# Kernel tuning notes

Hardware: AMD Instinct MI355X
Metric: run time of the kernel (lower is better)

## Reference

```python
import jax, jax.numpy as jnp
import numpy as np

B, SQ, SK, D = 8, 2048, 2048, 256

def setup_inputs() -> dict:
    key = jax.random.key(0)
    ks = jax.random.split(key, 8)
    x1 = jax.random.normal(ks[0], (B, SQ, D), dtype=jnp.float32)
    x2 = jax.random.normal(ks[1], (B, SK, D), dtype=jnp.float32)
    x3 = jax.random.normal(ks[2], (B, SK, D), dtype=jnp.float32)  # unused by the original forward (value=x3 is dead)
    mask = jax.random.bernoulli(ks[3], 0.8, (B, SK))
    scale = 0.02
    Wq = jax.random.normal(ks[4], (D, D), dtype=jnp.float32) * scale
    Wk = jax.random.normal(ks[5], (D, D), dtype=jnp.float32) * scale
    Wv = jax.random.normal(ks[6], (D, D), dtype=jnp.float32) * scale
    bq = jnp.zeros((D,), jnp.float32)
    bk = jnp.zeros((D,), jnp.float32)
    bv = jnp.zeros((D,), jnp.float32)
    return {"x1": x1, "x2": x2, "x3": x3, "Wq": Wq, "Wk": Wk, "Wv": Wv,
            "bq": bq, "bk": bk, "bv": bv, "mask": mask}

def reference(x1, x2, x3, Wq, Wk, Wv, bq, bk, bv, mask):
    d = x1.shape[-1]
    inv_sqrt_d = 1.0 / jnp.sqrt(jnp.asarray(d, x1.dtype))
    # Projections (single-head MHA with query scaling, as in torch MHA internals)
    q = (x1 @ Wq + bq) * inv_sqrt_d          # [B, SQ, D]
    k = x2 @ Wk + bk                          # [B, SK, D]
    v = x2 @ Wv + bv                          # forward_value(key): value projected from key input
    # Raw scores
    qk = jnp.einsum('bqd,bkd->bqk', q, k)     # [B, SQ, SK]
    # Mask-derived per-column rescale: qk /= (mask.size(0)/mask.sum(-2))**0.5
    m = mask.astype(qk.dtype)                 # [B, SK]
    col_count = jnp.sum(m, axis=0, keepdims=True)           # [1, SK]
    factor = jnp.sqrt(jnp.asarray(mask.shape[0], qk.dtype) / col_count)  # [1, SK]
    qk = qk / factor                          # broadcast over [B, SQ, SK]; div-by-inf -> 0 where column count is 0
    attn = jax.nn.softmax(qk, axis=-1)
    # dropout is identity in eval / p=0
    out = jnp.einsum('bqk,bkd->bqd', attn, v)  # [B, SQ, D]
    return out
```

## Files before the change

### kernel.cpp

```cpp
#include <hip/hip_runtime.h>
#include <hip/hip_bf16.h>
#include <math.h>

#define B_  8
#define SQ_ 2048
#define SK_ 2048
#define D_  256
#define NSPLIT 4
#define KEYS_PER_SPLIT (SK_ / NSPLIT)
#define NT (KEYS_PER_SPLIT / 32)

typedef __attribute__((ext_vector_type(8))) short bf16x8;
typedef __attribute__((ext_vector_type(4))) float f32x4;
typedef __attribute__((ext_vector_type(4))) unsigned short u16x4;
typedef __attribute__((ext_vector_type(8))) _Float16 f16x8;

static __device__ __forceinline__ unsigned short f2bf(float f) {
    unsigned int u = __builtin_bit_cast(unsigned int, f);
    u += 0x7FFFu + ((u >> 16) & 1u);
    return (unsigned short)(u >> 16);
}

static __device__ __forceinline__ void gld_lds16(const unsigned short* g, unsigned short* l) {
    __builtin_amdgcn_global_load_lds(
        (const __attribute__((address_space(1))) unsigned int*)g,
        (__attribute__((address_space(3))) unsigned int*)l, 16, 0, 0);
}

__global__ void prep_kernel(const float* __restrict__ Wq, const float* __restrict__ Wk,
                            const float* __restrict__ Wv, const int* __restrict__ mask,
                            unsigned short* __restrict__ wT, float* __restrict__ r) {
    int bid = blockIdx.x;
    if (bid < 768) {
        int p = bid >> 8, k = bid & 255, n = threadIdx.x;
        const float* W = (p == 0 ? Wq : (p == 1 ? Wk : Wv));
        wT[(size_t)p * D_ * D_ + (size_t)n * D_ + k] = f2bf(W[(size_t)k * D_ + n]);
    } else {
        int s = (bid - 768) * 256 + threadIdx.x;
        float c = 0.f;
#pragma unroll
        for (int b = 0; b < B_; b++) c += (mask[b * SK_ + s] != 0) ? 1.f : 0.f;
        r[s] = sqrtf(c * 0.125f);
    }
}

__global__ __launch_bounds__(256) void proj_kernel(
    const float* __restrict__ x1, const float* __restrict__ x2,
    const float* __restrict__ bq, const float* __restrict__ bk, const float* __restrict__ bv,
    const unsigned short* __restrict__ wT, const float* __restrict__ r,
    unsigned short* __restrict__ qb, unsigned short* __restrict__ kb,
    unsigned short* __restrict__ vt)
{
    __shared__ unsigned short xs[64][264];
    __shared__ unsigned short wsh[256][36];
    const int tid = threadIdx.x;
    const int mt = blockIdx.x, b = blockIdx.y, p = blockIdx.z;
    const int m0 = mt * 64;
    const float* x = (p == 0 ? x1 : x2) + (size_t)b * SQ_ * D_;

#pragma unroll
    for (int i = 0; i < 16; i++) {
        int id = tid + i * 256;
        int row = id >> 6, c4 = id & 63;
        float4 v = *(const float4*)(x + (size_t)(m0 + row) * D_ + c4 * 4);
        u16x4 u;
        u.x = f2bf(v.x); u.y = f2bf(v.y); u.z = f2bf(v.z); u.w = f2bf(v.w);
        *(u16x4*)(&xs[row][c4 * 4]) = u;
    }

    const int wv = tid >> 6, lane = tid & 63, l15 = lane & 15, quad = lane >> 4;
    const unsigned short* w = wT + (size_t)p * D_ * D_ + (size_t)tid * D_;

    f32x4 acc[4][4];
#pragma unroll
    for (int a = 0; a < 4; a++)
#pragma unroll
        for (int n = 0; n < 4; n++) acc[a][n] = (f32x4){0.f, 0.f, 0.f, 0.f};

    bf16x8 Wreg[4];
#pragma unroll
    for (int j = 0; j < 4; j++) Wreg[j] = *(const bf16x8*)(w + j * 8);

    for (int c = 0; c < 8; c++) {
        __syncthreads();
#pragma unroll
        for (int j = 0; j < 4; j++) *(bf16x8*)(&wsh[tid][j * 8]) = Wreg[j];
        if (c < 7) {
#pragma unroll
            for (int j = 0; j < 4; j++) Wreg[j] = *(const bf16x8*)(w + (c + 1) * 32 + j * 8);
        }
        __syncthreads();

        bf16x8 af[4];
#pragma unroll
        for (int a = 0; a < 4; a++)
            af[a] = *(const bf16x8*)(&xs[a * 16 + l15][c * 32 + quad * 8]);
#pragma unroll
        for (int nt = 0; nt < 4; nt++) {
            bf16x8 bfr = *(const bf16x8*)(&wsh[wv * 64 + nt * 16 + l15][quad * 8]);
#pragma unroll
            for (int a = 0; a < 4; a++)
                acc[a][nt] = __builtin_amdgcn_mfma_f32_16x16x32_bf16(af[a], bfr, acc[a][nt], 0, 0, 0);
        }
    }

    const float* bias = (p == 0 ? bq : (p == 1 ? bk : bv));
    if (p == 2) {
#pragma unroll
        for (int nt = 0; nt < 4; nt++) {
            int d = wv * 64 + nt * 16 + l15;
            float bb = bias[d];
#pragma unroll
            for (int a = 0; a < 4; a++) {
                int seqb = m0 + a * 16 + quad * 4;
                u16x4 u;
#pragma unroll
                for (int g = 0; g < 4; g++) u[g] = f2bf(acc[a][nt][g] + bb);
                *(u16x4*)(vt + ((size_t)b * D_ + d) * SK_ + seqb) = u;
            }
        }
    } else {
        unsigned short* dst = (p == 0 ? qb : kb);
#pragma unroll
        for (int a = 0; a < 4; a++) {
            int seqb = m0 + a * 16 + quad * 4;
            float rv[4];
#pragma unroll
            for (int g = 0; g < 4; g++)
                rv[g] = (p == 1) ? r[seqb + g] : 0.0625f;
#pragma unroll
            for (int nt = 0; nt < 4; nt++) {
                int col = wv * 64 + nt * 16 + l15;
                float bb = bias[col];
#pragma unroll
                for (int g = 0; g < 4; g++) {
                    float v = (acc[a][nt][g] + bb) * rv[g];
                    dst[((size_t)b * SQ_ + seqb + g) * D_ + col] = f2bf(v);
                }
            }
        }
    }
}

__global__ __launch_bounds__(256, 2) void flash_kernel(
    const unsigned short* __restrict__ qb, const unsigned short* __restrict__ kb,
    const unsigned short* __restrict__ vt, _Float16* __restrict__ Op,
    float* __restrict__ lp)
{
    __shared__ unsigned short Ks[2][32 * 256];
    __shared__ unsigned short Vs[2][256 * 32];
    __shared__ unsigned short Ps[4][32][40];
    const int tid = threadIdx.x;
    const int wv = tid >> 6, lane = tid & 63, l15 = lane & 15, quad = lane >> 4;
    const int bid = blockIdx.x;
    const int g = bid & 31, q = bid >> 5;
    const int b = g >> 2, sp = g & 3;
    const int q0 = q * 128 + wv * 32;

    const unsigned short* kbb = kb + ((size_t)b * SK_ + sp * KEYS_PER_SPLIT) * D_;
    const unsigned short* vtb = vt + (size_t)b * D_ * SK_ + sp * KEYS_PER_SPLIT;

    int krow[4], kck[4], vd[4], vch[4];
#pragma unroll
    for (int i = 0; i < 4; i++) {
        int id = i * 256 + tid;
        krow[i] = id >> 5; kck[i] = (id & 31) ^ (krow[i] & 7);
        vd[i] = id >> 2;   vch[i] = id & 3;
    }

#pragma unroll
    for (int i = 0; i < 4; i++)
        gld_lds16(kbb + (size_t)krow[i] * D_ + kck[i] * 8,
                  &Ks[0][(i * 256 + wv * 64) * 8]);
#pragma unroll
    for (int i = 0; i < 4; i++)
        gld_lds16(vtb + (size_t)vd[i] * SK_ + vch[i] * 8,
                  &Vs[0][(i * 256 + wv * 64) * 8]);

    bf16x8 qf[2][8];
#pragma unroll
    for (int mt = 0; mt < 2; mt++) {
        const unsigned short* qrow = qb + ((size_t)(b * SQ_ + q0 + mt * 16 + l15)) * D_;
#pragma unroll
        for (int c = 0; c < 8; c++)
            qf[mt][c] = *(const bf16x8*)(qrow + c * 32 + quad * 8);
    }

    f32x4 o[2][16];
#pragma unroll
    for (int mt = 0; mt < 2; mt++)
#pragma unroll
        for (int n = 0; n < 16; n++) o[mt][n] = (f32x4){0.f, 0.f, 0.f, 0.f};
    float l_[2][4] = {{0.f, 0.f, 0.f, 0.f}, {0.f, 0.f, 0.f, 0.f}};

    for (int kt = 0; kt < NT; kt++) {
        const int cur = kt & 1;
        __syncthreads();
        if (kt + 1 < NT) {
            const unsigned short* kn = kbb + (size_t)(kt + 1) * 32 * D_;
            const unsigned short* vn = vtb + (size_t)(kt + 1) * 32;
#pragma unroll
            for (int i = 0; i < 4; i++)
                gld_lds16(kn + (size_t)krow[i] * D_ + kck[i] * 8,
                          &Ks[cur ^ 1][(i * 256 + wv * 64) * 8]);
#pragma unroll
            for (int i = 0; i < 4; i++)
                gld_lds16(vn + (size_t)vd[i] * SK_ + vch[i] * 8,
                          &Vs[cur ^ 1][(i * 256 + wv * 64) * 8]);
        }

        f32x4 s[2][2];
        s[0][0] = (f32x4){0.f,0.f,0.f,0.f}; s[0][1] = (f32x4){0.f,0.f,0.f,0.f};
        s[1][0] = (f32x4){0.f,0.f,0.f,0.f}; s[1][1] = (f32x4){0.f,0.f,0.f,0.f};
#pragma unroll
        for (int h = 0; h < 2; h++)
#pragma unroll
            for (int c = 0; c < 8; c++) {
                bf16x8 kf = *(const bf16x8*)(
                    &Ks[cur][(h * 16 + l15) * 256 + (((c * 4 + quad) ^ (l15 & 7)) * 8)]);
                s[0][h] = __builtin_amdgcn_mfma_f32_16x16x32_bf16(qf[0][c], kf, s[0][h], 0, 0, 0);
                s[1][h] = __builtin_amdgcn_mfma_f32_16x16x32_bf16(qf[1][c], kf, s[1][h], 0, 0, 0);
            }

#pragma unroll
        for (int mt = 0; mt < 2; mt++)
#pragma unroll
            for (int h = 0; h < 2; h++)
#pragma unroll
                for (int g2 = 0; g2 < 4; g2++) {
                    float pv = __expf(s[mt][h][g2]);
                    l_[mt][g2] += pv;
                    Ps[wv][mt * 16 + quad * 4 + g2][h * 16 + l15] = f2bf(pv);
                }
        asm volatile("s_waitcnt lgkmcnt(0)" ::: "memory");

        bf16x8 pf0 = *(const bf16x8*)(&Ps[wv][l15][quad * 8]);
        bf16x8 pf1 = *(const bf16x8*)(&Ps[wv][16 + l15][quad * 8]);

#pragma unroll
        for (int n = 0; n < 16; n++) {
            bf16x8 vf = *(const bf16x8*)(&Vs[cur][(n * 16 + l15) * 32 + quad * 8]);
            o[0][n] = __builtin_amdgcn_mfma_f32_16x16x32_bf16(pf0, vf, o[0][n], 0, 0, 0);
            o[1][n] = __builtin_amdgcn_mfma_f32_16x16x32_bf16(pf1, vf, o[1][n], 0, 0, 0);
        }
    }

#pragma unroll
    for (int mt = 0; mt < 2; mt++)
#pragma unroll
        for (int g2 = 0; g2 < 4; g2++) {
            float t = l_[mt][g2];
            t += __shfl_xor(t, 1, 64);
            t += __shfl_xor(t, 2, 64);
            t += __shfl_xor(t, 4, 64);
            t += __shfl_xor(t, 8, 64);
            l_[mt][g2] = t;
        }

    _Float16* op = Op + ((size_t)(sp * B_ + b) * SQ_ + q0) * D_;
#pragma unroll
    for (int mt = 0; mt < 2; mt++)
#pragma unroll
        for (int g2 = 0; g2 < 4; g2++) {
            size_t ro = (size_t)(mt * 16 + quad * 4 + g2) * D_ + l15;
#pragma unroll
            for (int n = 0; n < 16; n++)
                op[ro + n * 16] = (_Float16)(o[mt][n][g2]);
        }
    if (l15 == 0) {
        float* lpp = lp + (size_t)(sp * B_ + b) * SQ_ + q0;
#pragma unroll
        for (int mt = 0; mt < 2; mt++)
#pragma unroll
            for (int g2 = 0; g2 < 4; g2++)
                lpp[mt * 16 + quad * 4 + g2] = l_[mt][g2];
    }
}

__global__ __launch_bounds__(256) void combine_kernel(
    const _Float16* __restrict__ Op, const float* __restrict__ lp,
    float* __restrict__ out)
{
    const int gid = blockIdx.x * 256 + threadIdx.x;
    const int row = gid >> 5;
    const size_t base = (size_t)gid * 8;
    float l = lp[row] + lp[B_ * SQ_ + row] + lp[2 * B_ * SQ_ + row] + lp[3 * B_ * SQ_ + row];
    float inv = 1.f / l;
    float acc[8] = {0,0,0,0,0,0,0,0};
#pragma unroll
    for (int sp = 0; sp < NSPLIT; sp++) {
        f16x8 v = *(const f16x8*)(Op + (size_t)sp * B_ * SQ_ * D_ + base);
#pragma unroll
        for (int j = 0; j < 8; j++) acc[j] += (float)v[j];
    }
    float4 r0 = {acc[0] * inv, acc[1] * inv, acc[2] * inv, acc[3] * inv};
    float4 r1 = {acc[4] * inv, acc[5] * inv, acc[6] * inv, acc[7] * inv};
    *(float4*)(out + base) = r0;
    *(float4*)(out + base + 4) = r1;
}

extern "C" void kernel_launch(void* const* d_in, const int* in_sizes, int n_in,
                              void* d_out, int out_size, void* d_ws, size_t ws_size,
                              hipStream_t stream)
{
    const float* x1 = (const float*)d_in[0];
    const float* x2 = (const float*)d_in[1];
    const float* Wq = (const float*)d_in[3];
    const float* Wk = (const float*)d_in[4];
    const float* Wv = (const float*)d_in[5];
    const float* bq = (const float*)d_in[6];
    const float* bk = (const float*)d_in[7];
    const float* bv = (const float*)d_in[8];
    const int*  mask = (const int*)d_in[9];
    float* out = (float*)d_out;

    char* ws = (char*)d_ws;
    unsigned short* qb = (unsigned short*)(ws);
    unsigned short* kb = (unsigned short*)(ws + 8388608);
    unsigned short* vt = (unsigned short*)(ws + 16777216);
    unsigned short* wT = (unsigned short*)(ws + 25165824);
    float*          r  = (float*)(ws + 25559040);
    float*          lp = (float*)(ws + 25567232);
    _Float16*       Op = (_Float16*)(ws + 25829376);

    prep_kernel<<<dim3(768 + SK_ / 256), 256, 0, stream>>>(Wq, Wk, Wv, mask, wT, r);
    proj_kernel<<<dim3(SQ_ / 64, B_, 3), 256, 0, stream>>>(x1, x2, bq, bk, bv, wT, r, qb, kb, vt);
    flash_kernel<<<dim3((SQ_ / 128) * B_ * NSPLIT), 256, 0, stream>>>(qb, kb, vt, Op, lp);
    combine_kernel<<<dim3((B_ * SQ_ * D_ / 8) / 256), 256, 0, stream>>>(Op, lp, out);
}
```

Before: 188.5 us.

## Rewrite projection as per-wave register GEMM and swizzle V tile in LDS

The projection kernel drops its shared-memory staging and block barriers. Each wave now computes a 16-row by 256-column tile with the activations held in registers, and reads the weight fragments straight from global memory (served from L2/L1). Separately, the flash kernel XOR-swizzles the V tile chunk layout in LDS to reduce bank conflicts on V fragment reads. The trade-off is more global weight traffic and higher register pressure in the projection, in exchange for removing LDS round trips and synchronisation.

```diff
diff --git a/kernel.cpp b/kernel.cpp
--- a/kernel.cpp
+++ b/kernel.cpp
@@ -30,13 +30,13 @@
 __global__ void prep_kernel(const float* __restrict__ Wq, const float* __restrict__ Wk,
                             const float* __restrict__ Wv, const int* __restrict__ mask,
                             unsigned short* __restrict__ wT, float* __restrict__ r) {
-    int bid = blockIdx.x;
+    int bid = blockIdx.x, tid = threadIdx.x;
     if (bid < 768) {
-        int p = bid >> 8, k = bid & 255, n = threadIdx.x;
+        int p = bid >> 8, k = bid & 255;
         const float* W = (p == 0 ? Wq : (p == 1 ? Wk : Wv));
-        wT[(size_t)p * D_ * D_ + (size_t)n * D_ + k] = f2bf(W[(size_t)k * D_ + n]);
+        wT[(size_t)p * D_ * D_ + (size_t)tid * D_ + k] = f2bf(W[(size_t)k * D_ + tid]);
     } else {
-        int s = (bid - 768) * 256 + threadIdx.x;
+        int s = (bid - 768) * 256 + tid;
         float c = 0.f;
 #pragma unroll
         for (int b = 0; b < B_; b++) c += (mask[b * SK_ + s] != 0) ? 1.f : 0.f;
@@ -51,92 +51,74 @@
     unsigned short* __restrict__ qb, unsigned short* __restrict__ kb,
     unsigned short* __restrict__ vt)
 {
-    __shared__ unsigned short xs[64][264];
-    __shared__ unsigned short wsh[256][36];
     const int tid = threadIdx.x;
-    const int mt = blockIdx.x, b = blockIdx.y, p = blockIdx.z;
-    const int m0 = mt * 64;
-    const float* x = (p == 0 ? x1 : x2) + (size_t)b * SQ_ * D_;
-
-#pragma unroll
-    for (int i = 0; i < 16; i++) {
-        int id = tid + i * 256;
-        int row = id >> 6, c4 = id & 63;
-        float4 v = *(const float4*)(x + (size_t)(m0 + row) * D_ + c4 * 4);
-        u16x4 u;
-        u.x = f2bf(v.x); u.y = f2bf(v.y); u.z = f2bf(v.z); u.w = f2bf(v.w);
-        *(u16x4*)(&xs[row][c4 * 4]) = u;
-    }
-
     const int wv = tid >> 6, lane = tid & 63, l15 = lane & 15, quad = lane >> 4;
-    const unsigned short* w = wT + (size_t)p * D_ * D_ + (size_t)tid * D_;
-
-    f32x4 acc[4][4];
-#pragma unroll
-    for (int a = 0; a < 4; a++)
-#pragma unroll
-        for (int n = 0; n < 4; n++) acc[a][n] = (f32x4){0.f, 0.f, 0.f, 0.f};
-
-    bf16x8 Wreg[4];
-#pragma unroll
-    for (int j = 0; j < 4; j++) Wreg[j] = *(const bf16x8*)(w + j * 8);
-
+    const int gw = blockIdx.x * 4 + wv;
+    const int p = gw >> 10;
+    const int idx = gw & 1023;
+    const int b = idx >> 7, s16 = idx & 127;
+    const int row = s16 * 16 + l15;
+
+    const float* x = (p == 0 ? x1 : x2) + ((size_t)b * SQ_ + row) * D_;
+    const unsigned short* wbase = wT + (size_t)p * D_ * D_;
+
+    float4 xa[8], xb[8];
+#pragma unroll
     for (int c = 0; c < 8; c++) {
-        __syncthreads();
-#pragma unroll
-        for (int j = 0; j < 4; j++) *(bf16x8*)(&wsh[tid][j * 8]) = Wreg[j];
-        if (c < 7) {
-#pragma unroll
-            for (int j = 0; j < 4; j++) Wreg[j] = *(const bf16x8*)(w + (c + 1) * 32 + j * 8);
-        }
-        __syncthreads();
-
-        bf16x8 af[4];
-#pragma unroll
-        for (int a = 0; a < 4; a++)
-            af[a] = *(const bf16x8*)(&xs[a * 16 + l15][c * 32 + quad * 8]);
-#pragma unroll
-        for (int nt = 0; nt < 4; nt++) {
-            bf16x8 bfr = *(const bf16x8*)(&wsh[wv * 64 + nt * 16 + l15][quad * 8]);
-#pragma unroll
-            for (int a = 0; a < 4; a++)
-                acc[a][nt] = __builtin_amdgcn_mfma_f32_16x16x32_bf16(af[a], bfr, acc[a][nt], 0, 0, 0);
+        xa[c] = *(const float4*)(x + c * 32 + quad * 8);
+        xb[c] = *(const float4*)(x + c * 32 + quad * 8 + 4);
+    }
+    bf16x8 af[8];
+#pragma unroll
+    for (int c = 0; c < 8; c++) {
+        bf16x8 t;
+        t[0] = (short)f2bf(xa[c].x); t[1] = (short)f2bf(xa[c].y);
+        t[2] = (short)f2bf(xa[c].z); t[3] = (short)f2bf(xa[c].w);
+        t[4] = (short)f2bf(xb[c].x); t[5] = (short)f2bf(xb[c].y);
+        t[6] = (short)f2bf(xb[c].z); t[7] = (short)f2bf(xb[c].w);
+        af[c] = t;
+    }
+
+    f32x4 acc[16];
+#pragma unroll
+    for (int n = 0; n < 16; n++) acc[n] = (f32x4){0.f, 0.f, 0.f, 0.f};
+
+#pragma unroll
+    for (int c = 0; c < 8; c++) {
+#pragma unroll
+        for (int nt = 0; nt < 16; nt++) {
+            bf16x8 wf = *(const bf16x8*)(wbase + (size_t)(nt * 16 + l15) * D_
+                                         + c * 32 + quad * 8);
+            acc[nt] = __builtin_amdgcn_mfma_f32_16x16x32_bf16(af[c], wf, acc[nt], 0, 0, 0);
         }
     }
 
     const float* bias = (p == 0 ? bq : (p == 1 ? bk : bv));
+    const int seqb = s16 * 16 + quad * 4;
     if (p == 2) {
 #pragma unroll
-        for (int nt = 0; nt < 4; nt++) {
-            int d = wv * 64 + nt * 16 + l15;
+        for (int nt = 0; nt < 16; nt++) {
+            int d = nt * 16 + l15;
             float bb = bias[d];
-#pragma unroll
-            for (int a = 0; a < 4; a++) {
-                int seqb = m0 + a * 16 + quad * 4;
-                u16x4 u;
-#pragma unroll
-                for (int g = 0; g < 4; g++) u[g] = f2bf(acc[a][nt][g] + bb);
-                *(u16x4*)(vt + ((size_t)b * D_ + d) * SK_ + seqb) = u;
-            }
+            u16x4 u;
+#pragma unroll
+            for (int g = 0; g < 4; g++) u[g] = f2bf(acc[nt][g] + bb);
+            *(u16x4*)(vt + ((size_t)b * D_ + d) * SK_ + seqb) = u;
         }
     } else {
         unsigned short* dst = (p == 0 ? qb : kb);
-#pragma unroll
-        for (int a = 0; a < 4; a++) {
-            int seqb = m0 + a * 16 + quad * 4;
-            float rv[4];
-#pragma unroll
-            for (int g = 0; g < 4; g++)
-                rv[g] = (p == 1) ? r[seqb + g] : 0.0625f;
-#pragma unroll
-            for (int nt = 0; nt < 4; nt++) {
-                int col = wv * 64 + nt * 16 + l15;
-                float bb = bias[col];
-#pragma unroll
-                for (int g = 0; g < 4; g++) {
-                    float v = (acc[a][nt][g] + bb) * rv[g];
-                    dst[((size_t)b * SQ_ + seqb + g) * D_ + col] = f2bf(v);
-                }
+        float rv[4];
+#pragma unroll
+        for (int g = 0; g < 4; g++)
+            rv[g] = (p == 1) ? r[seqb + g] : 0.0625f;
+#pragma unroll
+        for (int nt = 0; nt < 16; nt++) {
+            int col = nt * 16 + l15;
+            float bb = bias[col];
+#pragma unroll
+            for (int g = 0; g < 4; g++) {
+                float v = (acc[nt][g] + bb) * rv[g];
+                dst[((size_t)b * SQ_ + seqb + g) * D_ + col] = f2bf(v);
             }
         }
     }
@@ -165,17 +147,15 @@
     for (int i = 0; i < 4; i++) {
         int id = i * 256 + tid;
         krow[i] = id >> 5; kck[i] = (id & 31) ^ (krow[i] & 7);
-        vd[i] = id >> 2;   vch[i] = id & 3;
+        vd[i] = id >> 2;   vch[i] = (id & 3) ^ ((vd[i] >> 1) & 3);
     }
 
 #pragma unroll
     for (int i = 0; i < 4; i++)
-        gld_lds16(kbb + (size_t)krow[i] * D_ + kck[i] * 8,
-                  &Ks[0][(i * 256 + wv * 64) * 8]);
+        gld_lds16(kbb + (size_t)krow[i] * D_ + kck[i] * 8, &Ks[0][(i * 256 + wv * 64) * 8]);
 #pragma unroll
     for (int i = 0; i < 4; i++)
-        gld_lds16(vtb + (size_t)vd[i] * SK_ + vch[i] * 8,
-                  &Vs[0][(i * 256 + wv * 64) * 8]);
+        gld_lds16(vtb + (size_t)vd[i] * SK_ + vch[i] * 8, &Vs[0][(i * 256 + wv * 64) * 8]);
 
     bf16x8 qf[2][8];
 #pragma unroll
@@ -237,9 +217,10 @@
         bf16x8 pf0 = *(const bf16x8*)(&Ps[wv][l15][quad * 8]);
         bf16x8 pf1 = *(const bf16x8*)(&Ps[wv][16 + l15][quad * 8]);
 
+        const int vsw = ((quad ^ ((l15 >> 1) & 3)) * 8);
 #pragma unroll
         for (int n = 0; n < 16; n++) {
-            bf16x8 vf = *(const bf16x8*)(&Vs[cur][(n * 16 + l15) * 32 + quad * 8]);
+            bf16x8 vf = *(const bf16x8*)(&Vs[cur][(n * 16 + l15) * 32 + vsw]);
             o[0][n] = __builtin_amdgcn_mfma_f32_16x16x32_bf16(pf0, vf, o[0][n], 0, 0, 0);
             o[1][n] = __builtin_amdgcn_mfma_f32_16x16x32_bf16(pf1, vf, o[1][n], 0, 0, 0);
         }
@@ -324,7 +305,7 @@
     _Float16*       Op = (_Float16*)(ws + 25829376);
 
     prep_kernel<<<dim3(768 + SK_ / 256), 256, 0, stream>>>(Wq, Wk, Wv, mask, wT, r);
-    proj_kernel<<<dim3(SQ_ / 64, B_, 3), 256, 0, stream>>>(x1, x2, bq, bk, bv, wT, r, qb, kb, vt);
+    proj_kernel<<<dim3(768), 256, 0, stream>>>(x1, x2, bq, bk, bv, wT, r, qb, kb, vt);
     flash_kernel<<<dim3((SQ_ / 128) * B_ * NSPLIT), 256, 0, stream>>>(qb, kb, vt, Op, lp);
     combine_kernel<<<dim3((B_ * SQ_ * D_ / 8) / 256), 256, 0, stream>>>(Op, lp, out);
 }
```

Result: slower. 227.8 us (+20.8%).
